# Optimization experiments

Measured on AMD Instinct MI355X. Metric: run time of the kernel, lower is better.

The kernel has to match this reference:

```python
import jax, jax.numpy as jnp
import numpy as np
from jax import lax

# Module constants (from init_kwargs)
B, C = 2, 64            # batch, in_channel
H, W, D = 64, 64, 64    # size
GROUPS = 2


def setup_inputs() -> dict:
    key = jax.random.key(0)
    ks = jax.random.split(key, 4)
    x = jax.random.normal(ks[0], (B, H * W * D, C), dtype=jnp.float32)
    # TransverseConv: Conv3d(2, W*2, (H,3,3), pad (0,1,1)) -> weight (O,I,kD,kH,kW)
    w_t = jax.random.normal(ks[1], (W * GROUPS, GROUPS, H, 3, 3), dtype=jnp.float32) * 0.02
    b_t = jnp.zeros((W * GROUPS,), jnp.float32)
    # CoronalConv: Conv3d(2, W*2, (3,3,D), pad (1,1,0))
    w_c = jax.random.normal(ks[2], (W * GROUPS, GROUPS, 3, 3, D), dtype=jnp.float32) * 0.02
    b_c = jnp.zeros((W * GROUPS,), jnp.float32)
    # map: Conv3d(2C, C, 1) stored as dense (C, 2C)
    w_map = jax.random.normal(ks[3], (C, 2 * C), dtype=jnp.float32) * 0.02
    b_map = jnp.zeros((C,), jnp.float32)
    return {"x": x, "w_t": w_t, "b_t": b_t, "w_c": w_c, "b_c": b_c,
            "w_map": w_map, "b_map": b_map}


def _forward(x, w_t, b_t, w_c, b_c, w_map, b_map):
    Bx, N, Cx = x.shape
    xg = x.transpose(0, 2, 1).reshape(Bx, Cx, H, W, D)   # (B,C,H,W,D)
    shortcut = xg
    xr = xg.reshape(Bx * Cx // GROUPS, GROUPS, H, W, D)
    dn = ('NCDHW', 'OIDHW', 'NCDHW')
    # Transverse: kernel spans full H -> output (B*C/2, 2W, 1, W, D)
    tans = lax.conv_general_dilated(xr, w_t, (1, 1, 1), [(0, 0), (1, 1), (1, 1)],
                                    dimension_numbers=dn)
    tans = tans + b_t[None, :, None, None, None]
    tans = tans.reshape(Bx, Cx, W, W, D)                 # (B,C,W,W,D)
    # Coronal: kernel spans full D -> output (B*C/2, 2W, H, W, 1)
    cor = lax.conv_general_dilated(xr, w_c, (1, 1, 1), [(1, 1), (1, 1), (0, 0)],
                                   dimension_numbers=dn)
    cor = cor + b_c[None, :, None, None, None]
    cor = cor.reshape(Bx, Cx, W, H, W)                   # (B,C,W,H,W)
    t1 = tans.transpose(0, 1, 3, 2, 4)                   # (B,C,W,W,D)
    c1 = cor.transpose(0, 1, 4, 3, 2)                    # (B,C,W,H,W)
    f = jnp.matmul(c1, t1).transpose(0, 1, 3, 2, 4)      # (B,C,H,W,D)
    attn = jnp.matmul(cor, tans).transpose(0, 1, 3, 2, 4)  # (B,C,H,W,D)
    cat = jnp.concatenate([shortcut * f, attn], axis=1)  # (B,2C,H,W,D)
    mapped = jnp.einsum('bkhwd,ck->bchwd', cat, w_map) + b_map[None, :, None, None, None]
    out = jax.nn.gelu(mapped, approximate=False)         # torch nn.GELU = exact erf
    return out.reshape(Bx, Cx, -1).transpose(0, 2, 1)    # (B,N,C)


def reference(x, w_t, b_t, w_c, b_c, w_map, b_map):
    return _forward(x, w_t, b_t, w_c, b_c, w_map, b_map)
```

## Files before the change

### kernel.cpp

```cpp
#include <hip/hip_runtime.h>
#include <hip/hip_bf16.h>
#include <math.h>

#define HWD 262144

typedef __attribute__((ext_vector_type(8))) short bf16x8;
typedef __attribute__((ext_vector_type(16))) float f32x16;

__device__ inline unsigned short bfu(float f) {
    __hip_bfloat16 h = __float2bfloat16(f);
    return *reinterpret_cast<unsigned short*>(&h);
}

__global__ void k_prep(const float* __restrict__ w_t, const float* __restrict__ w_c,
                       const float* __restrict__ w_map,
                       __hip_bfloat16* __restrict__ A_t, __hip_bfloat16* __restrict__ A_c,
                       __hip_bfloat16* __restrict__ Wb) {
    int i = blockIdx.x * 256 + threadIdx.x;
    if (i < 147456) {
        int kk = i & 15, oc = (i >> 4) & 127, ks = i >> 11;
        int z4 = ks & 3, kq = ks >> 2;
        int g = kq / 9, tap = kq - 9 * g;
        int z = z4 * 16 + kk;
        A_t[i] = __float2bfloat16(w_t[((oc * 2 + g) * 64 + z) * 9 + tap]);
        A_c[i] = __float2bfloat16(w_c[((oc * 2 + g) * 9 + tap) * 64 + z]);
    }
    if (i < 8192) {
        Wb[i] = __float2bfloat16(w_map[i]);
    }
}

__device__ inline void pack_row_bf16(__hip_bfloat16* dst, const float* src) {
    unsigned short u[16];
#pragma unroll
    for (int j = 0; j < 16; ++j) u[j] = bfu(src[j]);
    uint4* q = reinterpret_cast<uint4*>(dst);
    q[0] = *reinterpret_cast<const uint4*>(&u[0]);
    q[1] = *reinterpret_cast<const uint4*>(&u[8]);
}

__global__ void k_trans_c(const float* __restrict__ x, __hip_bfloat16* __restrict__ Xc) {
    __shared__ unsigned short tile[256][68];
    int b = blockIdx.y;
    long n0 = (long)blockIdx.x * 256;
    int t = threadIdx.x;
    const float4* xp4 = (const float4*)(x + ((long)b * HWD + n0) * 64);
#pragma unroll
    for (int i = 0; i < 16; ++i) {
        int f4i = i * 256 + t;
        float4 v = xp4[f4i];
        int nl = f4i >> 4, c4 = (f4i & 15) * 4;
        ushort4 u;
        u.x = bfu(v.x); u.y = bfu(v.y); u.z = bfu(v.z); u.w = bfu(v.w);
        *(ushort4*)&tile[nl][c4] = u;
    }
    __syncthreads();
    int c = t >> 2, hwl = t & 3;
    int hw0 = blockIdx.x * 4;
    __hip_bfloat16* dst0 = Xc + (long)(b * 64 + c) * HWD + (long)(hw0 + hwl) * 16;
#pragma unroll
    for (int z4 = 0; z4 < 4; ++z4) {
        unsigned short u[16];
#pragma unroll
        for (int j = 0; j < 16; ++j) u[j] = tile[hwl * 64 + z4 * 16 + j][c];
        __hip_bfloat16* dst = dst0 + z4 * 65536;
        *(uint4*)dst = *(const uint4*)&u[0];
        *(uint4*)(dst + 8) = *(const uint4*)&u[8];
    }
}

__global__ void k_trans_t(const float* __restrict__ x, __hip_bfloat16* __restrict__ Xt) {
    __shared__ unsigned short tile[256][68];
    int b = blockIdx.y;
    int wd0 = blockIdx.x * 4;
    int t = threadIdx.x;
    const float* xb = x + (long)b * HWD * 64 + (long)wd0 * 64;
#pragma unroll
    for (int i = 0; i < 16; ++i) {
        int idx = i * 256 + t;
        int h = idx >> 6, f = idx & 63;
        float4 v = *(const float4*)(xb + (long)h * 262144 + f * 4);
        int wdl = f >> 4, c4 = (f & 15) * 4;
        ushort4 u;
        u.x = bfu(v.x); u.y = bfu(v.y); u.z = bfu(v.z); u.w = bfu(v.w);
        *(ushort4*)&tile[wdl * 64 + h][c4] = u;
    }
    __syncthreads();
    int c = t >> 2, wdl = t & 3;
    __hip_bfloat16* dst0 = Xt + (long)(b * 64 + c) * HWD + (long)(wd0 + wdl) * 16;
#pragma unroll
    for (int z4 = 0; z4 < 4; ++z4) {
        unsigned short u[16];
#pragma unroll
        for (int j = 0; j < 16; ++j) u[j] = tile[wdl * 64 + z4 * 16 + j][c];
        __hip_bfloat16* dst = dst0 + z4 * 65536;
        *(uint4*)dst = *(const uint4*)&u[0];
        *(uint4*)(dst + 8) = *(const uint4*)&u[8];
    }
}

__global__ __launch_bounds__(256, 3) void k_conv_mfma(
        const __hip_bfloat16* __restrict__ Xt, const __hip_bfloat16* __restrict__ At_,
        const float* __restrict__ bt, float* __restrict__ OutT,
        const __hip_bfloat16* __restrict__ Xc, const __hip_bfloat16* __restrict__ Ac_,
        const float* __restrict__ bcb, float* __restrict__ OutC) {
    int Lfull = blockIdx.x;
    int halfk = Lfull >> 11;
    int L = Lfull & 2047;
    const __hip_bfloat16* X = halfk ? Xc : Xt;
    const __hip_bfloat16* Aglob = halfk ? Ac_ : At_;
    const float* bias = halfk ? bcb : bt;
    float* Out = halfk ? OutC : OutT;

    int grp = (L & 7) * 8 + ((L >> 3) >> 5);
    int pt = (L >> 3) & 31;
    int b = grp >> 5, ch = grp & 31;
    int p0 = pt * 2;
    const short* Xg = (const short*)(X + ((long)(b * 64 + 2 * ch)) * HWD);
    const short* Ag = (const short*)Aglob;
    int t = threadIdx.x;
    int lane = t & 63, wv = t >> 6;
    int O0 = (wv >> 1) * 64;
    int N0 = (wv & 1) * 64;
    int lrow = lane & 31, lq = lane >> 5;

    __shared__ __align__(16) short Bsm[2][4][2][1024];

    f32x16 acc00 = {0}, acc01 = {0}, acc10 = {0}, acc11 = {0};

    int srow = t >> 1, shalf = t & 1;
    int spr = srow >> 6, sq = srow & 63;
    const uint4 zero4 = {0u, 0u, 0u, 0u};
    uint4 ld0, ld1, ld2, ld3;

    auto stage_load = [&](int kq) {
        int g = (kq >= 9) ? 1 : 0;
        int tap = kq - 9 * g;
        int r = tap / 3, s = tap - 3 * r;
        int pp = p0 + spr + r - 1, qq = sq + s - 1;
        bool ok = ((unsigned)pp < 64u) && ((unsigned)qq < 64u);
        const short* px = Xg + (long)g * HWD + (pp * 64 + qq) * 16 + shalf * 8;
        ld0 = ok ? *(const uint4*)(px)           : zero4;
        ld1 = ok ? *(const uint4*)(px + 65536)   : zero4;
        ld2 = ok ? *(const uint4*)(px + 131072)  : zero4;
        ld3 = ok ? *(const uint4*)(px + 196608)  : zero4;
    };
    auto stage_write = [&](int buf) {
        *(uint4*)&Bsm[buf][0][shalf][srow * 8] = ld0;
        *(uint4*)&Bsm[buf][1][shalf][srow * 8] = ld1;
        *(uint4*)&Bsm[buf][2][shalf][srow * 8] = ld2;
        *(uint4*)&Bsm[buf][3][shalf][srow * 8] = ld3;
    };

    stage_load(0);
    stage_write(0);
    __syncthreads();

    int buf = 0;
    for (int kq = 0; kq < 18; ++kq) {
        if (kq < 17) stage_load(kq + 1);
#pragma unroll
        for (int z4 = 0; z4 < 4; ++z4) {
            int ks = kq * 4 + z4;
            const short* Apk = Ag + ks * 2048 + (O0 + lrow) * 16 + lq * 8;
            uint4 a0u = *(const uint4*)(Apk);
            uint4 a1u = *(const uint4*)(Apk + 512);
            bf16x8 a0 = *(bf16x8*)&a0u;
            bf16x8 a1 = *(bf16x8*)&a1u;
            bf16x8 b0 = *(const bf16x8*)&Bsm[buf][z4][lq][(N0 + lrow) * 8];
            bf16x8 b1 = *(const bf16x8*)&Bsm[buf][z4][lq][(N0 + 32 + lrow) * 8];
            acc00 = __builtin_amdgcn_mfma_f32_32x32x16_bf16(a0, b0, acc00, 0, 0, 0);
            acc01 = __builtin_amdgcn_mfma_f32_32x32x16_bf16(a0, b1, acc01, 0, 0, 0);
            acc10 = __builtin_amdgcn_mfma_f32_32x32x16_bf16(a1, b0, acc10, 0, 0, 0);
            acc11 = __builtin_amdgcn_mfma_f32_32x32x16_bf16(a1, b1, acc11, 0, 0, 0);
        }
        if (kq < 17) {
            stage_write(buf ^ 1);
            __syncthreads();
            buf ^= 1;
        }
    }

    long base0 = ((long)(b * 64 + 2 * ch)) * HWD + (long)p0 * 64;
    int n0l = N0 + lrow, n1l = N0 + 32 + lrow;
    long noff0 = (long)(n0l >> 6) * 64 + (n0l & 63);
    long noff1 = (long)(n1l >> 6) * 64 + (n1l & 63);
#pragma unroll
    for (int reg = 0; reg < 16; ++reg) {
        int row = (reg & 3) + 8 * (reg >> 2) + 4 * lq;
        int oc0 = O0 + row, oc1 = O0 + 32 + row;
        long cb0 = base0 + (long)(oc0 >> 6) * HWD + (long)(oc0 & 63) * 4096;
        long cb1 = base0 + (long)(oc1 >> 6) * HWD + (long)(oc1 & 63) * 4096;
        float bs0 = bias[oc0], bs1 = bias[oc1];
        Out[cb0 + noff0] = acc00[reg] + bs0;
        Out[cb0 + noff1] = acc01[reg] + bs0;
        Out[cb1 + noff0] = acc10[reg] + bs1;
        Out[cb1 + noff1] = acc11[reg] + bs1;
    }
}

__global__ __launch_bounds__(256) void k_attn(const float* __restrict__ Cc,
        const float* __restrict__ T, __hip_bfloat16* __restrict__ At) {
    __shared__ __align__(16) __hip_bfloat16 Ms[64][72];
    __shared__ __align__(16) __hip_bfloat16 Ns[64][72];
    int L = blockIdx.x;
    int xcd = L & 7, j = L >> 3;
    int bc = xcd * 16 + (j >> 6), w2 = j & 63;
    const float* Ap = Cc + ((long)bc * 64 + w2) * 4096;
    const float* Bp = T + ((long)bc * 64 + w2) * 4096;
    int t = threadIdx.x;
#pragma unroll
    for (int i = 0; i < 4; ++i) {
        int f = i * 256 + t;
        int r = f >> 4, q4 = (f & 15) * 4;
        float4 v = *(const float4*)(Ap + r * 64 + q4);
        ushort4 u;
        u.x = bfu(v.x); u.y = bfu(v.y); u.z = bfu(v.z); u.w = bfu(v.w);
        *(ushort4*)&Ms[r][q4] = u;
        float4 w = *(const float4*)(Bp + r * 64 + q4);
        Ns[q4 + 0][r] = __float2bfloat16(w.x);
        Ns[q4 + 1][r] = __float2bfloat16(w.y);
        Ns[q4 + 2][r] = __float2bfloat16(w.z);
        Ns[q4 + 3][r] = __float2bfloat16(w.w);
    }
    __syncthreads();
    int lane = t & 63, wv = t >> 6;
    int lrow = lane & 31, lhalf = lane >> 5;
    int hq = wv >> 1, dq = wv & 1;
    f32x16 acc = {0};
#pragma unroll
    for (int ks = 0; ks < 4; ++ks) {
        bf16x8 a = *(const bf16x8*)&Ms[hq * 32 + lrow][ks * 16 + lhalf * 8];
        bf16x8 bfr = *(const bf16x8*)&Ns[dq * 32 + lrow][ks * 16 + lhalf * 8];
        acc = __builtin_amdgcn_mfma_f32_32x32x16_bf16(a, bfr, acc, 0, 0, 0);
    }
    __hip_bfloat16* Ao = At + (long)bc * HWD + w2 * 64 + dq * 32 + lrow;
#pragma unroll
    for (int reg = 0; reg < 16; ++reg) {
        int hh = hq * 32 + (reg & 3) + 8 * (reg >> 2) + 4 * lhalf;
        Ao[(long)hh * 4096] = __float2bfloat16(acc[reg]);
    }
}

__global__ __launch_bounds__(256, 2) void k_f(const float* __restrict__ Cc,
        const float* __restrict__ T, __hip_bfloat16* __restrict__ F) {
    __shared__ float As[16][64][8];
    __shared__ float Bs[16][8][68];
    int L = blockIdx.x;
    int xcd = L & 7, j = L >> 3;
    int bc = xcd * 16 + (j >> 3), wt = j & 7;
    const float* Ab = Cc + (long)bc * HWD + wt * 8;
    const float* Bb = T + (long)bc * HWD + wt * 8 * 64;
    int t = threadIdx.x;
    int w = t & 7, h2 = t >> 3;
    f32x16 p00 = {0}, p01 = {0}, p02 = {0}, p03 = {0};
    f32x16 p10 = {0}, p11 = {0}, p12 = {0}, p13 = {0};

    for (int w2c = 0; w2c < 4; ++w2c) {
        __syncthreads();
#pragma unroll
        for (int i = 0; i < 8; ++i) {
            int f = i * 256 + t;
            int half = f & 1, hh = (f >> 1) & 63, kk = f >> 7;
            float4 v = *(const float4*)(Ab + (long)(w2c * 16 + kk) * 4096 + hh * 64 + half * 4);
            *(float4*)&As[kk][hh][half * 4] = v;
        }
#pragma unroll
        for (int i = 0; i < 8; ++i) {
            int f = i * 256 + t;
            int d4 = f & 15, ww = (f >> 4) & 7, kk = f >> 7;
            float4 v = *(const float4*)(Bb + (long)(w2c * 16 + kk) * 4096 + ww * 64 + d4 * 4);
            *(float4*)&Bs[kk][ww][d4 * 4] = v;
        }
        __syncthreads();
        for (int kk = 0; kk < 16; ++kk) {
            float a0 = As[kk][h2][w];
            float a1 = As[kk][h2 + 32][w];
            const float* br = &Bs[kk][w][0];
#pragma unroll
            for (int i = 0; i < 16; ++i) {
                p00[i] = fmaf(a0, br[i], p00[i]);
                p01[i] = fmaf(a0, br[16 + i], p01[i]);
                p02[i] = fmaf(a0, br[32 + i], p02[i]);
                p03[i] = fmaf(a0, br[48 + i], p03[i]);
                p10[i] = fmaf(a1, br[i], p10[i]);
                p11[i] = fmaf(a1, br[16 + i], p11[i]);
                p12[i] = fmaf(a1, br[32 + i], p12[i]);
                p13[i] = fmaf(a1, br[48 + i], p13[i]);
            }
        }
    }
    __hip_bfloat16* Fp = F + (long)bc * HWD + (long)h2 * 4096 + (wt * 8 + w) * 64;
    float tmp[16];
#pragma unroll
    for (int i = 0; i < 16; ++i) tmp[i] = p00[i];
    pack_row_bf16(Fp, tmp);
#pragma unroll
    for (int i = 0; i < 16; ++i) tmp[i] = p01[i];
    pack_row_bf16(Fp + 16, tmp);
#pragma unroll
    for (int i = 0; i < 16; ++i) tmp[i] = p02[i];
    pack_row_bf16(Fp + 32, tmp);
#pragma unroll
    for (int i = 0; i < 16; ++i) tmp[i] = p03[i];
    pack_row_bf16(Fp + 48, tmp);
    __hip_bfloat16* Fq = Fp + 32L * 4096;
#pragma unroll
    for (int i = 0; i < 16; ++i) tmp[i] = p10[i];
    pack_row_bf16(Fq, tmp);
#pragma unroll
    for (int i = 0; i < 16; ++i) tmp[i] = p11[i];
    pack_row_bf16(Fq + 16, tmp);
#pragma unroll
    for (int i = 0; i < 16; ++i) tmp[i] = p12[i];
    pack_row_bf16(Fq + 32, tmp);
#pragma unroll
    for (int i = 0; i < 16; ++i) tmp[i] = p13[i];
    pack_row_bf16(Fq + 48, tmp);
}

__global__ __launch_bounds__(256, 3) void k_map(const float* __restrict__ x,
        const __hip_bfloat16* __restrict__ F, const __hip_bfloat16* __restrict__ At,
        const __hip_bfloat16* __restrict__ Wb, const float* __restrict__ b_map,
        float* __restrict__ out) {
    __shared__ float xs[2][16][257];
    __shared__ __hip_bfloat16 fa[2][16][264];

    int t = threadIdx.x;
    long n0 = (long)blockIdx.x * 256;
    int b = (int)(n0 >> 18);
    long nn0 = n0 & (HWD - 1);
    const float* xblk = x + n0 * 64;
    const __hip_bfloat16* Fb = F + (long)b * 64 * HWD + nn0;
    const __hip_bfloat16* Ab = At + (long)b * 64 * HWD + nn0;

    int lane = t & 63, wv = t >> 6;
    int lrow = lane & 31, lhalf = lane >> 5;

    const short* Wp = (const short*)Wb;
    bf16x8 wb0[8], wb1[8];
#pragma unroll
    for (int kc = 0; kc < 8; ++kc) {
        uint4 u0 = *(const uint4*)(Wp + lrow * 128 + kc * 16 + lhalf * 8);
        uint4 u1 = *(const uint4*)(Wp + (32 + lrow) * 128 + kc * 16 + lhalf * 8);
        wb0[kc] = *(bf16x8*)&u0;
        wb1[kc] = *(bf16x8*)&u1;
    }

    f32x16 acc00 = {0}, acc01 = {0}, acc10 = {0}, acc11 = {0};

    float4 xa, xb_, xc_, xd;
    uint4 fe, ff;
    int nrA = t >> 2, j4A = (t & 3) * 4;
    int rowF0 = t >> 5, segF0 = t & 31;
    int rowF1 = (256 + t) >> 5, segF1 = t & 31;

    auto load_chunk = [&](int kc) {
        if (kc < 4) {
            xa  = *(const float4*)(xblk + (nrA +   0) * 64 + kc * 16 + j4A);
            xb_ = *(const float4*)(xblk + (nrA +  64) * 64 + kc * 16 + j4A);
            xc_ = *(const float4*)(xblk + (nrA + 128) * 64 + kc * 16 + j4A);
            xd  = *(const float4*)(xblk + (nrA + 192) * 64 + kc * 16 + j4A);
            fe = *(const uint4*)(Fb + (long)(kc * 16 + rowF0) * HWD + segF0 * 8);
            ff = *(const uint4*)(Fb + (long)(kc * 16 + rowF1) * HWD + segF1 * 8);
        } else {
            fe = *(const uint4*)(Ab + (long)((kc - 4) * 16 + rowF0) * HWD + segF0 * 8);
            ff = *(const uint4*)(Ab + (long)((kc - 4) * 16 + rowF1) * HWD + segF1 * 8);
        }
    };
    auto write_chunk = [&](int kc, int buf) {
        if (kc < 4) {
            xs[buf][j4A + 0][nrA +   0] = xa.x;
            xs[buf][j4A + 1][nrA +   0] = xa.y;
            xs[buf][j4A + 2][nrA +   0] = xa.z;
            xs[buf][j4A + 3][nrA +   0] = xa.w;
            xs[buf][j4A + 0][nrA +  64] = xb_.x;
            xs[buf][j4A + 1][nrA +  64] = xb_.y;
            xs[buf][j4A + 2][nrA +  64] = xb_.z;
            xs[buf][j4A + 3][nrA +  64] = xb_.w;
            xs[buf][j4A + 0][nrA + 128] = xc_.x;
            xs[buf][j4A + 1][nrA + 128] = xc_.y;
            xs[buf][j4A + 2][nrA + 128] = xc_.z;
            xs[buf][j4A + 3][nrA + 128] = xc_.w;
            xs[buf][j4A + 0][nrA + 192] = xd.x;
            xs[buf][j4A + 1][nrA + 192] = xd.y;
            xs[buf][j4A + 2][nrA + 192] = xd.z;
            xs[buf][j4A + 3][nrA + 192] = xd.w;
        }
        *(uint4*)&fa[buf][rowF0][segF0 * 8] = fe;
        *(uint4*)&fa[buf][rowF1][segF1 * 8] = ff;
    };

    load_chunk(0);
    write_chunk(0, 0);
    __syncthreads();

#pragma unroll
    for (int kc = 0; kc < 8; ++kc) {
        int buf = kc & 1;
        if (kc < 7) load_chunk(kc + 1);
        unsigned short pv[16];
        if (kc < 4) {
#pragma unroll
            for (int k2 = 0; k2 < 16; ++k2) {
                float p = xs[buf][k2][t] * __bfloat162float(fa[buf][k2][t]);
                pv[k2] = bfu(p);
            }
        } else {
#pragma unroll
            for (int k2 = 0; k2 < 16; ++k2)
                pv[k2] = *reinterpret_cast<const unsigned short*>(&fa[buf][k2][t]);
        }
        unsigned lo0 = (unsigned)pv[0]  | ((unsigned)pv[1]  << 16);
        unsigned lo1 = (unsigned)pv[2]  | ((unsigned)pv[3]  << 16);
        unsigned lo2 = (unsigned)pv[4]  | ((unsigned)pv[5]  << 16);
        unsigned lo3 = (unsigned)pv[6]  | ((unsigned)pv[7]  << 16);
        unsigned hi0 = (unsigned)pv[8]  | ((unsigned)pv[9]  << 16);
        unsigned hi1 = (unsigned)pv[10] | ((unsigned)pv[11] << 16);
        unsigned hi2 = (unsigned)pv[12] | ((unsigned)pv[13] << 16);
        unsigned hi3 = (unsigned)pv[14] | ((unsigned)pv[15] << 16);
        int sl0 = lane & 31, sl1 = lane | 32;
        bool lowh = lane < 32;
        unsigned s00 = __shfl(hi0, sl0), s01 = __shfl(hi1, sl0);
        unsigned s02 = __shfl(hi2, sl0), s03 = __shfl(hi3, sl0);
        unsigned r00 = __shfl(lo0, sl1), r01 = __shfl(lo1, sl1);
        unsigned r02 = __shfl(lo2, sl1), r03 = __shfl(lo3, sl1);
        uint4 ua0, ua1;
        ua0.x = lowh ? lo0 : s00; ua0.y = lowh ? lo1 : s01;
        ua0.z = lowh ? lo2 : s02; ua0.w = lowh ? lo3 : s03;
        ua1.x = lowh ? r00 : hi0; ua1.y = lowh ? r01 : hi1;
        ua1.z = lowh ? r02 : hi2; ua1.w = lowh ? r03 : hi3;
        bf16x8 a0 = *(bf16x8*)&ua0;
        bf16x8 a1 = *(bf16x8*)&ua1;
        acc00 = __builtin_amdgcn_mfma_f32_32x32x16_bf16(a0, wb0[kc], acc00, 0, 0, 0);
        acc01 = __builtin_amdgcn_mfma_f32_32x32x16_bf16(a0, wb1[kc], acc01, 0, 0, 0);
        acc10 = __builtin_amdgcn_mfma_f32_32x32x16_bf16(a1, wb0[kc], acc10, 0, 0, 0);
        acc11 = __builtin_amdgcn_mfma_f32_32x32x16_bf16(a1, wb1[kc], acc11, 0, 0, 0);
        if (kc < 7) {
            write_chunk(kc + 1, buf ^ 1);
            __syncthreads();
        }
    }

    float bs0 = b_map[lrow];
    float bs1 = b_map[32 + lrow];
    const float inv_sqrt2 = 0.70710678118654752440f;
    float* ob = out + (n0 + wv * 64) * 64;
#pragma unroll
    for (int reg = 0; reg < 16; ++reg) {
        int nrow = (reg & 3) + 8 * (reg >> 2) + 4 * lhalf;
        float v00 = acc00[reg] + bs0;
        float v01 = acc01[reg] + bs1;
        float v10 = acc10[reg] + bs0;
        float v11 = acc11[reg] + bs1;
        v00 = 0.5f * v00 * (1.f + erff(v00 * inv_sqrt2));
        v01 = 0.5f * v01 * (1.f + erff(v01 * inv_sqrt2));
        v10 = 0.5f * v10 * (1.f + erff(v10 * inv_sqrt2));
        v11 = 0.5f * v11 * (1.f + erff(v11 * inv_sqrt2));
        ob[(long)nrow * 64 + lrow] = v00;
        ob[(long)nrow * 64 + 32 + lrow] = v01;
        ob[(long)(32 + nrow) * 64 + lrow] = v10;
        ob[(long)(32 + nrow) * 64 + 32 + lrow] = v11;
    }
}

extern "C" void kernel_launch(void* const* d_in, const int* in_sizes, int n_in,
                              void* d_out, int out_size, void* d_ws, size_t ws_size,
                              hipStream_t stream) {
    const float* x     = (const float*)d_in[0];
    const float* w_t   = (const float*)d_in[1];
    const float* b_t   = (const float*)d_in[2];
    const float* w_c   = (const float*)d_in[3];
    const float* b_c   = (const float*)d_in[4];
    const float* w_map = (const float*)d_in[5];
    const float* b_map = (const float*)d_in[6];
    float* out = (float*)d_out;
    float* ws = (float*)d_ws;

    __hip_bfloat16* Xc = (__hip_bfloat16*)ws;
    __hip_bfloat16* Xt = (__hip_bfloat16*)(ws + 16777216L);
    float* T = ws + 33554432L;
    float* Cc = out;
    __hip_bfloat16* A_t = (__hip_bfloat16*)(ws + 67108864L);
    __hip_bfloat16* A_c = (__hip_bfloat16*)(ws + 67182592L);
    __hip_bfloat16* Wb = (__hip_bfloat16*)(ws + 67256320L);
    __hip_bfloat16* At_bf = Xc;
    __hip_bfloat16* F_bf = Xt;

    hipLaunchKernelGGL(k_prep, dim3(576), dim3(256), 0, stream, w_t, w_c, w_map, A_t, A_c, Wb);
    hipLaunchKernelGGL(k_trans_c, dim3(1024, 2), dim3(256), 0, stream, x, Xc);
    hipLaunchKernelGGL(k_trans_t, dim3(1024, 2), dim3(256), 0, stream, x, Xt);
    hipLaunchKernelGGL(k_conv_mfma, dim3(4096), dim3(256), 0, stream,
                       Xt, A_t, b_t, T, Xc, A_c, b_c, Cc);
    hipLaunchKernelGGL(k_attn, dim3(8192), dim3(256), 0, stream, Cc, T, At_bf);
    hipLaunchKernelGGL(k_f, dim3(1024), dim3(256), 0, stream, Cc, T, F_bf);
    hipLaunchKernelGGL(k_map, dim3(2048), dim3(256), 0, stream, x, F_bf, At_bf, Wb, b_map, out);
}
```

Baseline: 734.7 us.

## Replace scalar FMA batched matmul in k_f with bf16 MFMA

The f-product kernel used to accumulate fp32 FMAs per thread across 64x64 tiles. It now converts the Cc and T tiles to bf16 while staging them into transposed shared-memory layouts. Each of 8 waves then runs a 64x64x16 product per chunk with 32x32x16 bf16 MFMA, and the block size doubles to 512. This aims to cut the ALU-bound FMA cost, at the price of bf16 rounding on inputs, scattered 2-byte shared stores and strided 2-byte global writes.

```diff
diff --git a/kernel.cpp b/kernel.cpp
--- a/kernel.cpp
+++ b/kernel.cpp
@@ -242,81 +242,61 @@
     }
 }
 
-__global__ __launch_bounds__(256, 2) void k_f(const float* __restrict__ Cc,
+__global__ __launch_bounds__(512, 4) void k_f(const float* __restrict__ Cc,
         const float* __restrict__ T, __hip_bfloat16* __restrict__ F) {
-    __shared__ float As[16][64][8];
-    __shared__ float Bs[16][8][68];
+    __shared__ __align__(16) __hip_bfloat16 As[8][64][24];
+    __shared__ __align__(16) __hip_bfloat16 Ns[8][64][24];
     int L = blockIdx.x;
     int xcd = L & 7, j = L >> 3;
     int bc = xcd * 16 + (j >> 3), wt = j & 7;
-    const float* Ab = Cc + (long)bc * HWD + wt * 8;
-    const float* Bb = T + (long)bc * HWD + wt * 8 * 64;
-    int t = threadIdx.x;
-    int w = t & 7, h2 = t >> 3;
-    f32x16 p00 = {0}, p01 = {0}, p02 = {0}, p03 = {0};
-    f32x16 p10 = {0}, p11 = {0}, p12 = {0}, p13 = {0};
+    const float* Ab = Cc + (long)bc * HWD;
+    const float* Bb = T + (long)bc * HWD;
+    int t = threadIdx.x;
+    int lane = t & 63, wv = t >> 6;
+    int lrow = lane & 31, lhalf = lane >> 5;
+    f32x16 acc00 = {0}, acc01 = {0}, acc10 = {0}, acc11 = {0};
 
     for (int w2c = 0; w2c < 4; ++w2c) {
         __syncthreads();
 #pragma unroll
-        for (int i = 0; i < 8; ++i) {
-            int f = i * 256 + t;
+        for (int i = 0; i < 4; ++i) {
+            int f = i * 512 + t;
             int half = f & 1, hh = (f >> 1) & 63, kk = f >> 7;
-            float4 v = *(const float4*)(Ab + (long)(w2c * 16 + kk) * 4096 + hh * 64 + half * 4);
-            *(float4*)&As[kk][hh][half * 4] = v;
-        }
-#pragma unroll
-        for (int i = 0; i < 8; ++i) {
-            int f = i * 256 + t;
+            float4 v = *(const float4*)(Ab + (long)(w2c * 16 + kk) * 4096 + hh * 64 + wt * 8 + half * 4);
+            As[half * 4 + 0][hh][kk] = __float2bfloat16(v.x);
+            As[half * 4 + 1][hh][kk] = __float2bfloat16(v.y);
+            As[half * 4 + 2][hh][kk] = __float2bfloat16(v.z);
+            As[half * 4 + 3][hh][kk] = __float2bfloat16(v.w);
+        }
+#pragma unroll
+        for (int i = 0; i < 4; ++i) {
+            int f = i * 512 + t;
             int d4 = f & 15, ww = (f >> 4) & 7, kk = f >> 7;
-            float4 v = *(const float4*)(Bb + (long)(w2c * 16 + kk) * 4096 + ww * 64 + d4 * 4);
-            *(float4*)&Bs[kk][ww][d4 * 4] = v;
+            float4 v = *(const float4*)(Bb + (long)(w2c * 16 + kk) * 4096 + (wt * 8 + ww) * 64 + d4 * 4);
+            Ns[ww][d4 * 4 + 0][kk] = __float2bfloat16(v.x);
+            Ns[ww][d4 * 4 + 1][kk] = __float2bfloat16(v.y);
+            Ns[ww][d4 * 4 + 2][kk] = __float2bfloat16(v.z);
+            Ns[ww][d4 * 4 + 3][kk] = __float2bfloat16(v.w);
         }
         __syncthreads();
-        for (int kk = 0; kk < 16; ++kk) {
-            float a0 = As[kk][h2][w];
-            float a1 = As[kk][h2 + 32][w];
-            const float* br = &Bs[kk][w][0];
-#pragma unroll
-            for (int i = 0; i < 16; ++i) {
-                p00[i] = fmaf(a0, br[i], p00[i]);
-                p01[i] = fmaf(a0, br[16 + i], p01[i]);
-                p02[i] = fmaf(a0, br[32 + i], p02[i]);
-                p03[i] = fmaf(a0, br[48 + i], p03[i]);
-                p10[i] = fmaf(a1, br[i], p10[i]);
-                p11[i] = fmaf(a1, br[16 + i], p11[i]);
-                p12[i] = fmaf(a1, br[32 + i], p12[i]);
-                p13[i] = fmaf(a1, br[48 + i], p13[i]);
-            }
-        }
-    }
-    __hip_bfloat16* Fp = F + (long)bc * HWD + (long)h2 * 4096 + (wt * 8 + w) * 64;
-    float tmp[16];
-#pragma unroll
-    for (int i = 0; i < 16; ++i) tmp[i] = p00[i];
-    pack_row_bf16(Fp, tmp);
-#pragma unroll
-    for (int i = 0; i < 16; ++i) tmp[i] = p01[i];
-    pack_row_bf16(Fp + 16, tmp);
-#pragma unroll
-    for (int i = 0; i < 16; ++i) tmp[i] = p02[i];
-    pack_row_bf16(Fp + 32, tmp);
-#pragma unroll
-    for (int i = 0; i < 16; ++i) tmp[i] = p03[i];
-    pack_row_bf16(Fp + 48, tmp);
-    __hip_bfloat16* Fq = Fp + 32L * 4096;
-#pragma unroll
-    for (int i = 0; i < 16; ++i) tmp[i] = p10[i];
-    pack_row_bf16(Fq, tmp);
-#pragma unroll
-    for (int i = 0; i < 16; ++i) tmp[i] = p11[i];
-    pack_row_bf16(Fq + 16, tmp);
-#pragma unroll
-    for (int i = 0; i < 16; ++i) tmp[i] = p12[i];
-    pack_row_bf16(Fq + 32, tmp);
-#pragma unroll
-    for (int i = 0; i < 16; ++i) tmp[i] = p13[i];
-    pack_row_bf16(Fq + 48, tmp);
+        bf16x8 a0 = *(const bf16x8*)&As[wv][lrow][lhalf * 8];
+        bf16x8 a1 = *(const bf16x8*)&As[wv][32 + lrow][lhalf * 8];
+        bf16x8 b0 = *(const bf16x8*)&Ns[wv][lrow][lhalf * 8];
+        bf16x8 b1 = *(const bf16x8*)&Ns[wv][32 + lrow][lhalf * 8];
+        acc00 = __builtin_amdgcn_mfma_f32_32x32x16_bf16(a0, b0, acc00, 0, 0, 0);
+        acc01 = __builtin_amdgcn_mfma_f32_32x32x16_bf16(a0, b1, acc01, 0, 0, 0);
+        acc10 = __builtin_amdgcn_mfma_f32_32x32x16_bf16(a1, b0, acc10, 0, 0, 0);
+        acc11 = __builtin_amdgcn_mfma_f32_32x32x16_bf16(a1, b1, acc11, 0, 0, 0);
+    }
+    __hip_bfloat16* Fp = F + (long)bc * HWD + (wt * 8 + wv) * 64;
+#pragma unroll
+    for (int reg = 0; reg < 16; ++reg) {
+        int row = (reg & 3) + 8 * (reg >> 2) + 4 * lhalf;
+        Fp[(long)row * 4096 + lrow]             = __float2bfloat16(acc00[reg]);
+        Fp[(long)row * 4096 + 32 + lrow]        = __float2bfloat16(acc01[reg]);
+        Fp[(long)(32 + row) * 4096 + lrow]      = __float2bfloat16(acc10[reg]);
+        Fp[(long)(32 + row) * 4096 + 32 + lrow] = __float2bfloat16(acc11[reg]);
+    }
 }
 
 __global__ __launch_bounds__(256, 3) void k_map(const float* __restrict__ x,
@@ -493,6 +473,6 @@
     hipLaunchKernelGGL(k_conv_mfma, dim3(4096), dim3(256), 0, stream,
                        Xt, A_t, b_t, T, Xc, A_c, b_c, Cc);
     hipLaunchKernelGGL(k_attn, dim3(8192), dim3(256), 0, stream, Cc, T, At_bf);
-    hipLaunchKernelGGL(k_f, dim3(1024), dim3(256), 0, stream, Cc, T, F_bf);
+    hipLaunchKernelGGL(k_f, dim3(1024), dim3(512), 0, stream, Cc, T, F_bf);
     hipLaunchKernelGGL(k_map, dim3(2048), dim3(256), 0, stream, x, F_bf, At_bf, Wb, b_map, out);
 }
```

Result: faster. 714.0 us (-2.8%).
